# Performance work log

Measured on AMD Instinct MI355X. Metric: run time of the kernel, lower is better.

Reference implementation:

```python
import jax, jax.numpy as jnp
import numpy as np

N, IN_CH, OUT_CH = 2, 16, 32
SPATIAL = (20, 20, 20, 20)
KER = (3, 3, 3, 3)


def setup_inputs() -> dict:
    key = jax.random.key(0)
    kx, kw = jax.random.split(key)
    x = jax.random.normal(kx, (N, IN_CH) + SPATIAL, dtype=jnp.float32)
    # kaiming-uniform-like init scale; exact init distribution irrelevant for correctness baseline
    fan_in = IN_CH * int(np.prod(KER))
    bound = float(np.sqrt(6.0 / fan_in))
    w = jax.random.uniform(kw, (IN_CH, OUT_CH) + KER, dtype=jnp.float32,
                           minval=-bound, maxval=bound)
    return {"x": x, "w": w}


def reference(x, w):
    # x: [n, in_ch, d1, d2, d3, d4]; w: [in_ch, out_ch, k1, k2, k3, k4]
    # valid 4D convolution (cross-correlation), stride 1 -- same math as the
    # torch as_strided im2col + tensordot, but expressed as a sum over the
    # (small, fixed) kernel offsets to avoid materializing the im2col tensor.
    kd = w.shape[2:]
    od = tuple(x.shape[2 + i] - kd[i] + 1 for i in range(4))  # output spatial dims
    out = jnp.zeros((x.shape[0], w.shape[1]) + od, dtype=x.dtype)
    for a in range(kd[0]):
        for b in range(kd[1]):
            for c in range(kd[2]):
                for d in range(kd[3]):
                    patch = x[:, :, a:a + od[0], b:b + od[1], c:c + od[2], d:d + od[3]]
                    out = out + jnp.einsum('ncijkl,co->noijkl', patch, w[:, :, a, b, c, d])
    return out
```

## Files before the change

### kernel.cpp

```cpp
#include <hip/hip_runtime.h>


typedef unsigned short ushort_t;
typedef __attribute__((ext_vector_type(8)))  __bf16 bf16x8;
typedef __attribute__((ext_vector_type(16))) float  f32x16;
typedef __attribute__((ext_vector_type(4)))  unsigned int uint4v;

__device__ __forceinline__ ushort_t f2bf(float f) {
    union { float f; unsigned int u; } v; v.f = f;
    unsigned int r = v.u + 0x7FFFu + ((v.u >> 16) & 1u);
    return (ushort_t)(r >> 16);
}

__device__ __forceinline__ void gload16(const ushort_t* g, ushort_t* l) {
    __builtin_amdgcn_global_load_lds(
        (const __attribute__((address_space(1))) unsigned int*)g,
        (__attribute__((address_space(3))) unsigned int*)l, 16, 0, 0);
}

__global__ __launch_bounds__(256) void prepass(const float* __restrict__ x,
                                               const float* __restrict__ w,
                                               ushort_t* __restrict__ xt,
                                               ushort_t* __restrict__ wt) {
    const int blk = blockIdx.x;
    if (blk < 1250) {
        const int g = blk * 256 + threadIdx.x;
        const int n = g / 160000, rem = g % 160000;
        const float* xs = x + (size_t)n * 2560000 + rem;
        unsigned int pk[8];
        #pragma unroll
        for (int e = 0; e < 8; ++e) {
            unsigned int lo = f2bf(xs[(size_t)(2 * e) * 160000]);
            unsigned int hi = f2bf(xs[(size_t)(2 * e + 1) * 160000]);
            pk[e] = lo | (hi << 16);
        }
        uint4v* q = (uint4v*)xt + (size_t)g * 2;
        uint4v q0; q0[0] = pk[0]; q0[1] = pk[1]; q0[2] = pk[2]; q0[3] = pk[3];
        uint4v q1; q1[0] = pk[4]; q1[1] = pk[5]; q1[2] = pk[6]; q1[3] = pk[7];
        q[0] = q0; q[1] = q1;
    } else {
        const int s = (blk - 1250) * 256 + threadIdx.x;
        if (s < 41472) {
            const int ic = s / 2592, rem = s % 2592;
            const int oc = rem / 81, tap = rem % 81;
            wt[tap * 512 + (ic >> 3) * 256 + oc * 8 + (ic & 7)] = f2bf(w[s]);
        }
    }
}

__global__ __launch_bounds__(256, 4) void conv4d_mfma(
    const ushort_t* __restrict__ xt, const ushort_t* __restrict__ wt,
    float* __restrict__ out)
{
    __shared__ ushort_t lwt[2][4608];

    const int wgid = blockIdx.x;
    const int g = (wgid & 7) * 243 + (wgid >> 3);
    const int n = g / 972;
    int rem = g - n * 972;
    const int j = rem / 54;  rem -= j * 54;
    const int i = rem / 3;
    const int q = rem - i * 3;

    const int t = threadIdx.x;
    const int lane = t & 63, wv = t >> 6;
    const int col = lane & 31, ic8 = lane >> 5;

    const int T = q * 4 + wv;
    const int sp = T * 30 + col;
    const int spc = sp > 359 ? 359 : sp;
    const int cb = spc * 32 + ic8 * 16;
    const int aoffB = ic8 * 512 + col * 16;

    f32x16 acc0, acc1, acc2;
    #pragma unroll
    for (int r = 0; r < 16; ++r) { acc0[r] = 0.0f; acc1[r] = 0.0f; acc2[r] = 0.0f; }

    const char* xnij = (const char*)(xt + (size_t)n * 2560000
                                        + (size_t)i * 128000 + (size_t)j * 6400);

    {
        const ushort_t* gw = wt;
        gload16(gw + t * 8,        lwt[0] + (wv << 9));
        gload16(gw + 2048 + t * 8, lwt[0] + 2048 + (wv << 9));
        if (t < 64) gload16(gw + 4096 + t * 8, lwt[0] + 4096);
    }

    for (int ab = 0; ab < 9; ++ab) {
        __syncthreads();

        if (ab < 8) {
            const ushort_t* gw = wt + (size_t)(ab + 1) * 4608;
            ushort_t* lw = lwt[(ab + 1) & 1];
            gload16(gw + t * 8,        lw + (wv << 9));
            gload16(gw + 2048 + t * 8, lw + 2048 + (wv << 9));
            if (t < 64) gload16(gw + 4096 + t * 8, lw + 4096);
        }

        const int a = ab / 3, b = ab % 3;
        const char* xs = xnij + ((size_t)a * 128000 + (size_t)b * 6400) * 2;
        const char* wbase = (const char*)lwt[ab & 1];
        #pragma unroll
        for (int c = 0; c < 3; ++c) {
            bf16x8 af0 = *(const bf16x8*)(wbase + (c * 3 + 0) * 1024 + aoffB);
            bf16x8 af1 = *(const bf16x8*)(wbase + (c * 3 + 1) * 1024 + aoffB);
            bf16x8 af2 = *(const bf16x8*)(wbase + (c * 3 + 2) * 1024 + aoffB);
            bf16x8 bv  = *(const bf16x8*)(xs + cb + c * 640);
            acc0 = __builtin_amdgcn_mfma_f32_32x32x16_bf16(af0, bv, acc0, 0, 0, 0);
            acc1 = __builtin_amdgcn_mfma_f32_32x32x16_bf16(af1, bv, acc1, 0, 0, 0);
            acc2 = __builtin_amdgcn_mfma_f32_32x32x16_bf16(af2, bv, acc2, 0, 0, 0);
        }
    }

    const int s = sp;
    const int k = s / 20, ls = s % 20;
    const bool val = (col <= 29) && (ls <= 17) && (s <= 357);
    float* po = out + (size_t)n * 3359232 + (size_t)i * 5832 + (size_t)j * 324
                    + (size_t)ic8 * 419904 + k * 18 + ls;
    const int src1 = (lane & 32) | ((col + 1) & 31);
    const int src2 = (lane & 32) | ((col + 2) & 31);

    #pragma unroll
    for (int r = 0; r < 16; ++r) {
        const float v1 = __shfl(acc1[r], src1, 64);
        const float v2 = __shfl(acc2[r], src2, 64);
        const float res = acc0[r] + v1 + v2;
        const int offr = ((r & 3) + 8 * (r >> 2)) * 104976;
        if (val) po[offr] = res;
    }
}

extern "C" void kernel_launch(void* const* d_in, const int* in_sizes, int n_in,
                              void* d_out, int out_size, void* d_ws, size_t ws_size,
                              hipStream_t stream) {
    const float* x = (const float*)d_in[0];
    const float* w = (const float*)d_in[1];
    float* out = (float*)d_out;

    ushort_t* xt = (ushort_t*)d_ws;
    ushort_t* wt = (ushort_t*)((char*)d_ws + (size_t)10240000);

    prepass<<<dim3(1412), 256, 0, stream>>>(x, w, xt, wt);
    conv4d_mfma<<<dim3(1944), 256, 0, stream>>>(xt, wt, out);
}
```

Baseline: 40.84 us.

## Process three spatial tiles per wave to reuse weight fragments across MFMAs

Each workgroup now covers all 12 spatial row-tiles of an (n,i,j) slab instead of 4. Each wave handles three tiles, so the weight fragments read from LDS and the staged weight loads serve three times as many MFMAs. The grid drops from 1944 to 648 blocks and occupancy is lowered to 2 blocks per SM because there are now nine 16-float accumulators per thread. The cost is more register pressure, fewer concurrent waves to hide global-load latency, and a grid that may underfill the 256 CUs.

```diff
diff --git a/kernel.cpp b/kernel.cpp
--- a/kernel.cpp
+++ b/kernel.cpp
@@ -48,33 +48,38 @@
     }
 }
 
-__global__ __launch_bounds__(256, 4) void conv4d_mfma(
+__global__ __launch_bounds__(256, 2) void conv4d_mfma(
     const ushort_t* __restrict__ xt, const ushort_t* __restrict__ wt,
     float* __restrict__ out)
 {
     __shared__ ushort_t lwt[2][4608];
 
     const int wgid = blockIdx.x;
-    const int g = (wgid & 7) * 243 + (wgid >> 3);
-    const int n = g / 972;
-    int rem = g - n * 972;
-    const int j = rem / 54;  rem -= j * 54;
-    const int i = rem / 3;
-    const int q = rem - i * 3;
+    const int tile_ = (wgid & 7) * 81 + (wgid >> 3);
+    const int n = tile_ / 324;
+    const int rem_ = tile_ - n * 324;
+    const int j = rem_ / 18, i = rem_ % 18;
 
     const int t = threadIdx.x;
     const int lane = t & 63, wv = t >> 6;
     const int col = lane & 31, ic8 = lane >> 5;
 
-    const int T = q * 4 + wv;
-    const int sp = T * 30 + col;
-    const int spc = sp > 359 ? 359 : sp;
-    const int cb = spc * 32 + ic8 * 16;
+    int sp[3]; int cb[3];
+    #pragma unroll
+    for (int m = 0; m < 3; ++m) {
+        sp[m] = (3 * wv + m) * 30 + col;
+        const int spc = sp[m] > 359 ? 359 : sp[m];
+        cb[m] = spc * 32 + ic8 * 16;
+    }
     const int aoffB = ic8 * 512 + col * 16;
 
-    f32x16 acc0, acc1, acc2;
+    f32x16 acc[3][3];
     #pragma unroll
-    for (int r = 0; r < 16; ++r) { acc0[r] = 0.0f; acc1[r] = 0.0f; acc2[r] = 0.0f; }
+    for (int d = 0; d < 3; ++d)
+        #pragma unroll
+        for (int m = 0; m < 3; ++m)
+            #pragma unroll
+            for (int r = 0; r < 16; ++r) acc[d][m][r] = 0.0f;
 
     const char* xnij = (const char*)(xt + (size_t)n * 2560000
                                         + (size_t)i * 128000 + (size_t)j * 6400);
@@ -105,28 +110,35 @@
             bf16x8 af0 = *(const bf16x8*)(wbase + (c * 3 + 0) * 1024 + aoffB);
             bf16x8 af1 = *(const bf16x8*)(wbase + (c * 3 + 1) * 1024 + aoffB);
             bf16x8 af2 = *(const bf16x8*)(wbase + (c * 3 + 2) * 1024 + aoffB);
-            bf16x8 bv  = *(const bf16x8*)(xs + cb + c * 640);
-            acc0 = __builtin_amdgcn_mfma_f32_32x32x16_bf16(af0, bv, acc0, 0, 0, 0);
-            acc1 = __builtin_amdgcn_mfma_f32_32x32x16_bf16(af1, bv, acc1, 0, 0, 0);
-            acc2 = __builtin_amdgcn_mfma_f32_32x32x16_bf16(af2, bv, acc2, 0, 0, 0);
+            #pragma unroll
+            for (int m = 0; m < 3; ++m) {
+                bf16x8 bv = *(const bf16x8*)(xs + cb[m] + c * 640);
+                acc[0][m] = __builtin_amdgcn_mfma_f32_32x32x16_bf16(af0, bv, acc[0][m], 0, 0, 0);
+                acc[1][m] = __builtin_amdgcn_mfma_f32_32x32x16_bf16(af1, bv, acc[1][m], 0, 0, 0);
+                acc[2][m] = __builtin_amdgcn_mfma_f32_32x32x16_bf16(af2, bv, acc[2][m], 0, 0, 0);
+            }
         }
     }
 
-    const int s = sp;
-    const int k = s / 20, ls = s % 20;
-    const bool val = (col <= 29) && (ls <= 17) && (s <= 357);
-    float* po = out + (size_t)n * 3359232 + (size_t)i * 5832 + (size_t)j * 324
-                    + (size_t)ic8 * 419904 + k * 18 + ls;
+    float* outb = out + (size_t)n * 3359232 + (size_t)i * 5832 + (size_t)j * 324
+                      + (size_t)ic8 * 419904;
     const int src1 = (lane & 32) | ((col + 1) & 31);
     const int src2 = (lane & 32) | ((col + 2) & 31);
 
     #pragma unroll
-    for (int r = 0; r < 16; ++r) {
-        const float v1 = __shfl(acc1[r], src1, 64);
-        const float v2 = __shfl(acc2[r], src2, 64);
-        const float res = acc0[r] + v1 + v2;
-        const int offr = ((r & 3) + 8 * (r >> 2)) * 104976;
-        if (val) po[offr] = res;
+    for (int m = 0; m < 3; ++m) {
+        const int s = sp[m];
+        const int k = s / 20, ls = s % 20;
+        const bool val = (col <= 29) && (ls <= 17) && (s <= 357);
+        float* po = outb + k * 18 + ls;
+        #pragma unroll
+        for (int r = 0; r < 16; ++r) {
+            const float v1 = __shfl(acc[1][m][r], src1, 64);
+            const float v2 = __shfl(acc[2][m][r], src2, 64);
+            const float res = acc[0][m][r] + v1 + v2;
+            const int offr = ((r & 3) + 8 * (r >> 2)) * 104976;
+            if (val) po[offr] = res;
+        }
     }
 }
 
@@ -141,5 +153,5 @@
     ushort_t* wt = (ushort_t*)((char*)d_ws + (size_t)10240000);
 
     prepass<<<dim3(1412), 256, 0, stream>>>(x, w, xt, wt);
-    conv4d_mfma<<<dim3(1944), 256, 0, stream>>>(xt, wt, out);
+    conv4d_mfma<<<dim3(648), 256, 0, stream>>>(xt, wt, out);
 }
```

After: 44.92 us. 10.0% more time.
